# Performance work log

Hardware: AMD Instinct MI355X
Metric: run time of the kernel (lower is better)

Reference implementation:

```python
import jax, jax.numpy as jnp
import numpy as np

B, D1, SN, NF = 32, 49, 32, 16          # batch, n_sais, sqrt_n, n_filters
D_MODEL, HEADS = SN * SN * NF, 16        # 16384, 16
DEPTH = D_MODEL // HEADS                 # 1024
C_IN = 16


def setup_inputs() -> dict:
    key = jax.random.key(0)
    ks = jax.random.split(key, 11)
    mk = lambda k, shape, scale=1.0: jax.random.normal(k, shape, dtype=jnp.float32) * scale
    w_scale = 1.0 / np.sqrt(C_IN)
    return {
        "v": mk(ks[0], (B, D1, SN, SN, C_IN)),
        "k": mk(ks[1], (B, D1, SN, SN, C_IN)),
        "q": mk(ks[2], (B, D1, SN, SN, C_IN)),
        # 1x1x1 Conv3D == pointwise channel matmul: weight [C_in, n_filters] + bias
        "Wq": mk(ks[3], (C_IN, NF), w_scale), "bq": jnp.zeros((NF,), jnp.float32),
        "Wk": mk(ks[4], (C_IN, NF), w_scale), "bk": jnp.zeros((NF,), jnp.float32),
        "Wv": mk(ks[5], (C_IN, NF), w_scale), "bv": jnp.zeros((NF,), jnp.float32),
        "Wo": mk(ks[6], (NF, NF), w_scale),   "bo": jnp.zeros((NF,), jnp.float32),
    }


def _pointwise(x, W, b):
    # Conv3D(kernel=1, padding='same') over [B, d1, h, w, c]
    return jnp.einsum('bdhwc,cf->bdhwf', x, W) + b


def reference(v, k, q, Wq, bq, Wk, bk, Wv, bv, Wo, bo):
    b = q.shape[0]
    # projections (1x1x1 conv3d), then flatten spatial+channel into d_model
    def proj_heads(x, W, bias):
        y = _pointwise(x, W, bias).reshape(b, D1, D_MODEL)       # reshape2d
        y = y.reshape(b, D1, HEADS, DEPTH)                        # split_heads
        return y.transpose(0, 2, 1, 3)                            # [b, h, d1, depth]
    qh = proj_heads(q, Wq, bq)
    kh = proj_heads(k, Wk, bk)
    vh = proj_heads(v, Wv, bv)
    # scaled dot-product attention over the 49 SAI tokens
    scale = 1.0 / jnp.sqrt(jnp.float32(DEPTH))
    scores = jnp.einsum('bhqd,bhkd->bhqk', qh, kh) * scale        # [b, h, 49, 49]
    attn = jax.nn.softmax(scores, axis=-1)
    ctx = jnp.einsum('bhqk,bhkd->bhqd', attn, vh)                 # [b, h, 49, depth]
    ctx = ctx.transpose(0, 2, 1, 3).reshape(b, D1, D_MODEL)       # concat heads
    ctx = ctx.reshape(b, D1, SN, SN, NF)                          # reshape4d
    out = _pointwise(ctx, Wo, bo)                                 # wout conv3d 1x1x1
    return out, attn
```

## Files before the change

### kernel.cpp

```cpp
#include <hip/hip_runtime.h>
#include <hip/hip_bf16.h>


#define NT 49
#define TOKS 16384
#define HSL 1024
#define SLOT 3200
#define ZSWZ(n) (((((n) & 7) ^ (((n) >> 3) & 7))) << 4)
#define SW64(t) (((t) & 7) << 4)

typedef __attribute__((ext_vector_type(8))) short bf16x8;
typedef __attribute__((ext_vector_type(4))) float f32x4;

__device__ __forceinline__ ushort f2bf(float f) {
    union { float f; unsigned u; } v; v.f = f;
    return (ushort)((v.u + 0x7fffu + ((v.u >> 16) & 1u)) >> 16);
}
__device__ __forceinline__ unsigned pk2(float lo, float hi) {
    return (unsigned)f2bf(lo) | ((unsigned)f2bf(hi) << 16);
}
__device__ __forceinline__ float qdot(f32x4 x0, f32x4 x1, f32x4 x2, f32x4 x3,
                                      f32x4 wa, f32x4 wb, f32x4 wc, f32x4 wd) {
    float s =      x0[0]*wa[0];
    s = fmaf(x0[1], wa[1], s); s = fmaf(x0[2], wa[2], s); s = fmaf(x0[3], wa[3], s);
    s = fmaf(x1[0], wb[0], s); s = fmaf(x1[1], wb[1], s); s = fmaf(x1[2], wb[2], s);
    s = fmaf(x1[3], wb[3], s);
    s = fmaf(x2[0], wc[0], s); s = fmaf(x2[1], wc[1], s); s = fmaf(x2[2], wc[2], s);
    s = fmaf(x2[3], wc[3], s);
    s = fmaf(x3[0], wd[0], s); s = fmaf(x3[1], wd[1], s); s = fmaf(x3[2], wd[2], s);
    s = fmaf(x3[3], wd[3], s);
    return s;
}

#define W_DECL(mb) \
    f32x4 W00 = *(const f32x4*)((mb)+ 0), W01 = *(const f32x4*)((mb)+ 4), \
          W02 = *(const f32x4*)((mb)+ 8), W03 = *(const f32x4*)((mb)+12), \
          W10 = *(const f32x4*)((mb)+16), W11 = *(const f32x4*)((mb)+20), \
          W12 = *(const f32x4*)((mb)+24), W13 = *(const f32x4*)((mb)+28), \
          W20 = *(const f32x4*)((mb)+32), W21 = *(const f32x4*)((mb)+36), \
          W22 = *(const f32x4*)((mb)+40), W23 = *(const f32x4*)((mb)+44), \
          W30 = *(const f32x4*)((mb)+48), W31 = *(const f32x4*)((mb)+52), \
          W32 = *(const f32x4*)((mb)+56), W33 = *(const f32x4*)((mb)+60)

__global__ __launch_bounds__(256, 2) void k_scores8(
    const float* __restrict__ qin, const float* __restrict__ kin,
    const float* __restrict__ Wq, const float* __restrict__ bq,
    const float* __restrict__ Wk, float* __restrict__ ws1)
{
    __shared__ ushort bufA[64*64];
    __shared__ ushort bufB[64*64];
    __shared__ float  Msh[256];
    __shared__ float  wkbqSh[16];
    __shared__ float  gSh[64];

    const int tid  = threadIdx.x;
    const int lane = tid & 63;
    const int wv   = tid >> 6;
    const int s    = blockIdx.x & 7;
    const int h    = (blockIdx.x >> 3) & 15;
    const int b    = blockIdx.x >> 7;

    const float* qbase = qin + (size_t)b*NT*TOKS + h*HSL + s*128;
    const float* kbase = kin + (size_t)b*NT*TOKS + h*HSL + s*128;

    const int f4 = tid & 31;
    const int t0 = tid >> 5;
    const int si = (tid >> 2) & 7;
    const int rq = tid & 3;

    f32x4 kv[7];
    {
        const float* kp = kbase + f4*4;
        #pragma unroll
        for (int i = 0; i < 7; ++i) {
            const int t = t0 + 8*i; const int tc = t < 48 ? t : 48;
            kv[i] = *(const f32x4*)(kp + (size_t)tc*TOKS);
        }
    }
    f32x4 q0[7], q1[7], q2[7], q3[7];
    #pragma unroll
    for (int i = 0; i < 7; ++i) {
        const int t = t0 + 8*i; const int tc = t < 48 ? t : 48;
        const float* qc = qbase + si*16 + (size_t)tc*TOKS;
        q0[i] = *(const f32x4*)(qc);
        q1[i] = *(const f32x4*)(qc + 4);
        q2[i] = *(const f32x4*)(qc + 8);
        q3[i] = *(const f32x4*)(qc + 12);
    }

    {
        unsigned* zA = (unsigned*)bufA; unsigned* zB = (unsigned*)bufB;
        #pragma unroll
        for (int i = 0; i < 2; ++i) {
            const int j = tid + 256*i;
            if (j < 480) { zA[1568 + j] = 0u; zB[1568 + j] = 0u; }
        }
        const int c1 = tid >> 4, c2 = tid & 15;
        float m = 0.f;
        #pragma unroll
        for (int f = 0; f < 16; ++f) m += Wq[c1*16+f] * Wk[c2*16+f];
        Msh[c2*16 + c1] = m;
        if (tid < 16) {
            float wb = 0.f;
            #pragma unroll
            for (int g = 0; g < 16; ++g) wb += Wk[tid*16+g] * bq[g];
            wkbqSh[tid] = wb;
        }
        if (tid < 64) gSh[tid] = 0.f;
    }
    __syncthreads();

    W_DECL(Msh + rq*64);
    const f32x4 wkb = *(const f32x4*)(wkbqSh + (f4 & 3)*4);

    uint2 kw[7];
    #pragma unroll
    for (int i = 0; i < 7; ++i) {
        const int t = t0 + 8*i;
        f32x4 xk = kv[i];
        if (t >= NT) xk = (f32x4){0.f,0.f,0.f,0.f};
        kw[i].x = pk2(xk[0], xk[1]); kw[i].y = pk2(xk[2], xk[3]);
        const float pg = xk[0]*wkb[0] + xk[1]*wkb[1] + xk[2]*wkb[2] + xk[3]*wkb[3];
        if (pg != 0.f) atomicAdd(&gSh[t], pg);
    }
    uint2 qw[7];
    #pragma unroll
    for (int i = 0; i < 7; ++i) {
        const float o0 = qdot(q0[i],q1[i],q2[i],q3[i], W00,W01,W02,W03);
        const float o1 = qdot(q0[i],q1[i],q2[i],q3[i], W10,W11,W12,W13);
        const float o2 = qdot(q0[i],q1[i],q2[i],q3[i], W20,W21,W22,W23);
        const float o3 = qdot(q0[i],q1[i],q2[i],q3[i], W30,W31,W32,W33);
        qw[i].x = pk2(o0, o1); qw[i].y = pk2(o2, o3);
    }

    const int f4h = f4 >> 4, f4l = f4 & 15;
    const int sih = si >> 2, sil = si & 3;
    const int ra  = wv*16 + (lane & 15);

    f32x4 accS[4];
    #pragma unroll
    for (int nt = 0; nt < 4; ++nt) accS[nt] = (f32x4){0.f,0.f,0.f,0.f};

    #pragma unroll
    for (int h2 = 0; h2 < 2; ++h2) {
        if (f4h == h2) {
            #pragma unroll
            for (int i = 0; i < 7; ++i) {
                const int t = t0 + 8*i;
                *(uint2*)((char*)bufB + ((t*128 + f4l*8) ^ SW64(t))) = kw[i];
            }
        }
        if (sih == h2) {
            #pragma unroll
            for (int i = 0; i < 7; ++i) {
                const int t = t0 + 8*i;
                if (t < NT)
                    *(uint2*)((char*)bufA + ((t*128 + sil*32 + rq*8) ^ SW64(t))) = qw[i];
            }
        }
        __syncthreads();
        #pragma unroll
        for (int ks2 = 0; ks2 < 2; ++ks2) {
            const int abo = (ra*128 + ks2*64 + (lane >> 4)*16) ^ SW64(ra);
            const bf16x8 af = *(const bf16x8*)((const char*)bufA + abo);
            #pragma unroll
            for (int nt = 0; nt < 4; ++nt) {
                const int rb  = nt*16 + (lane & 15);
                const int bbo = (rb*128 + ks2*64 + (lane >> 4)*16) ^ SW64(rb);
                const bf16x8 bf = *(const bf16x8*)((const char*)bufB + bbo);
                accS[nt] = __builtin_amdgcn_mfma_f32_16x16x32_bf16(af, bf, accS[nt], 0, 0, 0);
            }
        }
        if (h2 == 0) __syncthreads();
    }

    float* slot = ws1 + (size_t)blockIdx.x * SLOT;
    #pragma unroll
    for (int nt = 0; nt < 4; ++nt) {
        const int col = nt*16 + (lane & 15);
        #pragma unroll
        for (int rr = 0; rr < 4; ++rr) {
            const int row = wv*16 + (lane >> 4)*4 + rr;
            if (row < NT) slot[row*64 + col] = accS[nt][rr];
        }
    }
    if (tid < 64) slot[3136 + tid] = gSh[tid];
}

template<int SPLIT, int LOG2S>
__global__ __launch_bounds__(256, 2) void k_scores(
    const float* __restrict__ qin, const float* __restrict__ kin,
    const float* __restrict__ Wq, const float* __restrict__ bq,
    const float* __restrict__ Wk, float* __restrict__ ws1)
{
    __shared__ ushort bufA[64*128];
    __shared__ ushort bufB[64*128];
    __shared__ float  Msh[256];
    __shared__ float  wkbqSh[16];
    __shared__ float  gSh[64];

    const int tid  = threadIdx.x;
    const int lane = tid & 63;
    const int wv   = tid >> 6;
    const int s    = blockIdx.x & (SPLIT - 1);
    const int h    = (blockIdx.x >> LOG2S) & 15;
    const int b    = blockIdx.x >> (LOG2S + 4);

    const float* qbase = qin + (size_t)b*NT*TOKS + h*HSL + s*(1024/SPLIT);
    const float* kbase = kin + (size_t)b*NT*TOKS + h*HSL + s*(1024/SPLIT);

    const int f4 = tid & 31;
    const int t0 = tid >> 5;
    const int si = (tid >> 2) & 7;
    const int rq = tid & 3;

    constexpr int NC = 8 / SPLIT;

    f32x4 kv[7];
    {
        const float* kp = kbase + f4*4;
        #pragma unroll
        for (int i = 0; i < 7; ++i) {
            const int t = t0 + 8*i; const int tc = t < 48 ? t : 48;
            kv[i] = *(const f32x4*)(kp + (size_t)tc*TOKS);
        }
    }
    f32x4 xa0, xa1, xa2, xa3;
    {
        const float* qc = qbase + si*16 + (size_t)t0*TOKS;
        xa0 = *(const f32x4*)(qc);
        xa1 = *(const f32x4*)(qc + 4);
        xa2 = *(const f32x4*)(qc + 8);
        xa3 = *(const f32x4*)(qc + 12);
    }

    {
        unsigned* z0 = (unsigned*)bufA; unsigned* z1 = (unsigned*)bufB;
        #pragma unroll
        for (int i = 0; i < 16; ++i) { z0[tid + 256*i] = 0u; z1[tid + 256*i] = 0u; }
        const int c1 = tid >> 4, c2 = tid & 15;
        float m = 0.f;
        #pragma unroll
        for (int f = 0; f < 16; ++f) m += Wq[c1*16+f] * Wk[c2*16+f];
        Msh[c2*16 + c1] = m;
        if (tid < 16) {
            float wb = 0.f;
            #pragma unroll
            for (int g = 0; g < 16; ++g) wb += Wk[tid*16+g] * bq[g];
            wkbqSh[tid] = wb;
        }
        if (tid < 64) gSh[tid] = 0.f;
    }
    __syncthreads();

    W_DECL(Msh + rq*64);
    f32x4 wkb = *(const f32x4*)(wkbqSh + (f4 & 3)*4);

    f32x4 accS[4];
    #pragma unroll
    for (int nt = 0; nt < 4; ++nt) accS[nt] = (f32x4){0.f,0.f,0.f,0.f};

    for (int kc = 0; kc < NC; ++kc) {
        if (kc > 0) {
            const float* kp = kbase + kc*128 + f4*4;
            #pragma unroll
            for (int i = 0; i < 7; ++i) {
                const int t = t0 + 8*i; const int tc = t < 48 ? t : 48;
                kv[i] = *(const f32x4*)(kp + (size_t)tc*TOKS);
            }
            const float* qc = qbase + kc*128 + si*16 + (size_t)t0*TOKS;
            xa0 = *(const f32x4*)(qc);
            xa1 = *(const f32x4*)(qc + 4);
            xa2 = *(const f32x4*)(qc + 8);
            xa3 = *(const f32x4*)(qc + 12);
        }
        #pragma unroll
        for (int i = 0; i < 7; ++i) {
            const int t = t0 + 8*i;
            f32x4 xk = kv[i];
            if (t >= NT) xk = (f32x4){0.f,0.f,0.f,0.f};
            uint2 w; w.x = pk2(xk[0], xk[1]); w.y = pk2(xk[2], xk[3]);
            *(uint2*)((char*)bufB + ((t*256 + f4*8) ^ ((t & 7) << 4))) = w;
            const float pg = xk[0]*wkb[0] + xk[1]*wkb[1] + xk[2]*wkb[2] + xk[3]*wkb[3];
            if (pg != 0.f) atomicAdd(&gSh[t], pg);
        }
        #pragma unroll
        for (int i = 0; i < 7; ++i) {
            f32x4 xb0 = xa0, xb1 = xa1, xb2 = xa2, xb3 = xa3;
            if (i < 6) {
                const int tn = t0 + 8*(i+1); const int tc = tn < 48 ? tn : 48;
                const float* qc = qbase + kc*128 + si*16 + (size_t)tc*TOKS;
                xb0 = *(const f32x4*)(qc);
                xb1 = *(const f32x4*)(qc + 4);
                xb2 = *(const f32x4*)(qc + 8);
                xb3 = *(const f32x4*)(qc + 12);
            }
            const int t = t0 + 8*i;
            if (t < NT) {
                const float o0 = qdot(xa0,xa1,xa2,xa3, W00,W01,W02,W03);
                const float o1 = qdot(xa0,xa1,xa2,xa3, W10,W11,W12,W13);
                const float o2 = qdot(xa0,xa1,xa2,xa3, W20,W21,W22,W23);
                const float o3 = qdot(xa0,xa1,xa2,xa3, W30,W31,W32,W33);
                uint2 w; w.x = pk2(o0, o1); w.y = pk2(o2, o3);
                *(uint2*)((char*)bufA + ((t*256 + si*32 + rq*8) ^ ((t & 7) << 4))) = w;
            }
            xa0 = xb0; xa1 = xb1; xa2 = xb2; xa3 = xb3;
        }
        __syncthreads();
        #pragma unroll
        for (int ks = 0; ks < 4; ++ks) {
            const int ra  = wv*16 + (lane & 15);
            const int abo = (ra*256 + (ks*32 + (lane >> 4)*8)*2) ^ ((ra & 7) << 4);
            const bf16x8 af = *(const bf16x8*)((const char*)bufA + abo);
            #pragma unroll
            for (int nt = 0; nt < 4; ++nt) {
                const int rb  = nt*16 + (lane & 15);
                const int bbo = (rb*256 + (ks*32 + (lane >> 4)*8)*2) ^ ((rb & 7) << 4);
                const bf16x8 bf = *(const bf16x8*)((const char*)bufB + bbo);
                accS[nt] = __builtin_amdgcn_mfma_f32_16x16x32_bf16(af, bf, accS[nt], 0, 0, 0);
            }
        }
        if (kc + 1 < NC) __syncthreads();
    }

    float* slot = ws1 + (size_t)blockIdx.x * SLOT;
    #pragma unroll
    for (int nt = 0; nt < 4; ++nt) {
        const int col = nt*16 + (lane & 15);
        #pragma unroll
        for (int rr = 0; rr < 4; ++rr) {
            const int row = wv*16 + (lane >> 4)*4 + rr;
            if (row < NT) slot[row*64 + col] = accS[nt][rr];
        }
    }
    if (tid < 64) slot[3136 + tid] = gSh[tid];
}

template<int SPLIT>
__global__ __launch_bounds__(256, 2) void k_softmax(
    const float* __restrict__ ws1, float* __restrict__ attnp,
    ushort* __restrict__ ws2)
{
    __shared__ float sS[NT*69];
    __shared__ float sG[64];
    const int tid = threadIdx.x;
    const float* base = ws1 + (size_t)blockIdx.x * SPLIT * SLOT;

    for (int p = tid; p < 784; p += 256) {
        const int row = p >> 4, c4 = (p & 15) * 4;
        float4 acc = *(const float4*)(base + row*64 + c4);
        #pragma unroll
        for (int s = 1; s < SPLIT; ++s) {
            const float4 a = *(const float4*)(base + s*SLOT + row*64 + c4);
            acc.x += a.x; acc.y += a.y; acc.z += a.z; acc.w += a.w;
        }
        sS[row*69 + c4 + 0] = acc.x;
        sS[row*69 + c4 + 1] = acc.y;
        sS[row*69 + c4 + 2] = acc.z;
        sS[row*69 + c4 + 3] = acc.w;
    }
    if (tid < 64) {
        float g = base[3136 + tid];
        #pragma unroll
        for (int s = 1; s < SPLIT; ++s) g += base[s*SLOT + 3136 + tid];
        sG[tid] = g;
    }
    __syncthreads();

    if (tid < NT) {
        float mx = -1e30f;
        for (int j = 0; j < NT; ++j) {
            const float v = (sS[tid*69 + j] + sG[j]) * 0.03125f;
            sS[tid*69 + j] = v;
            mx = fmaxf(mx, v);
        }
        float ssum = 0.f;
        for (int j = 0; j < NT; ++j) {
            const float e = __expf(sS[tid*69 + j] - mx);
            sS[tid*69 + j] = e; ssum += e;
        }
        const float inv = 1.0f / ssum;
        for (int j = 0; j < NT; ++j) sS[tid*69 + j] *= inv;
    }
    __syncthreads();

    float* ab = attnp + (size_t)blockIdx.x * (NT*NT);
    for (int p = tid; p < NT*NT; p += 256) {
        const int t = p / NT, j = p - t*NT;
        ab[p] = sS[t*69 + j];
    }
    ushort* w2 = ws2 + (size_t)blockIdx.x * 4096;
    for (int p = tid; p < 4096; p += 256) {
        const int t = p >> 6, j = p & 63;
        const float v = (t < NT && j < NT) ? sS[t*69 + j] : 0.f;
        w2[p] = f2bf(v);
    }
}

__global__ __launch_bounds__(256, 2) void k_out(
    const float* __restrict__ vin,
    const float* __restrict__ Wv, const float* __restrict__ bv,
    const float* __restrict__ Wo, const float* __restrict__ bo,
    const ushort* __restrict__ ws2, float* __restrict__ out)
{
    __shared__ unsigned Zt[4096];
    __shared__ float WvoSh[256];
    __shared__ float bvoSh[16];

    const int tid  = threadIdx.x;
    const int lane = tid & 63;
    const int wv   = tid >> 6;
    const int kc   = blockIdx.x & 7;
    const int h    = (blockIdx.x >> 3) & 15;
    const int b    = blockIdx.x >> 7;
    const float* vbase = vin + (size_t)b*NT*TOKS + h*HSL;

    const int si = (tid >> 2) & 7;
    const int rq = tid & 3;
    const int t0 = tid >> 5;

    const ushort* w2 = ws2 + ((size_t)(blockIdx.x >> 3)) * 4096;
    const int ra = wv*16 + (lane & 15);
    const bf16x8 af0 = *(const bf16x8*)(w2 + ra*64 +      (lane >> 4)*8);
    const bf16x8 af1 = *(const bf16x8*)(w2 + ra*64 + 32 + (lane >> 4)*8);
    f32x4 v0[7], v1[7], v2[7], v3[7];
    #pragma unroll
    for (int i = 0; i < 7; ++i) {
        const int t = t0 + 8*i; const int tc = t < 48 ? t : 48;
        const float* vc = vbase + kc*128 + si*16 + (size_t)tc*TOKS;
        v0[i] = *(const f32x4*)(vc);
        v1[i] = *(const f32x4*)(vc + 4);
        v2[i] = *(const f32x4*)(vc + 8);
        v3[i] = *(const f32x4*)(vc + 12);
    }

    {
        const int c1 = tid >> 4, c2 = tid & 15;
        float wvo = 0.f;
        #pragma unroll
        for (int f = 0; f < 16; ++f) wvo += Wv[c1*16+f] * Wo[f*16+c2];
        WvoSh[c2*16 + c1] = wvo;
        if (tid < 16) {
            float s2 = 0.f;
            #pragma unroll
            for (int g = 0; g < 16; ++g) s2 += bv[g]*Wo[g*16+tid];
            bvoSh[tid] = s2 + bo[tid];
        }
        #pragma unroll
        for (int i = 0; i < 16; ++i) Zt[tid + 256*i] = 0u;
    }
    __syncthreads();

    W_DECL(WvoSh + rq*64);
    const float bias = bvoSh[lane & 15];

    #pragma unroll
    for (int i = 0; i < 7; ++i) {
        const int t = t0 + 8*i;
        if (t < NT) {
            const float o0 = qdot(v0[i],v1[i],v2[i],v3[i], W00,W01,W02,W03);
            const float o1 = qdot(v0[i],v1[i],v2[i],v3[i], W10,W11,W12,W13);
            const float o2 = qdot(v0[i],v1[i],v2[i],v3[i], W20,W21,W22,W23);
            const float o3 = qdot(v0[i],v1[i],v2[i],v3[i], W30,W31,W32,W33);
            const int n0 = si*16 + rq*4;
            const int pb = (t >> 1)*4, hb = (t & 1)*2;
            *(ushort*)((char*)Zt + ((((n0+0)*128 + pb) ^ ZSWZ(n0+0)) + hb)) = f2bf(o0);
            *(ushort*)((char*)Zt + ((((n0+1)*128 + pb) ^ ZSWZ(n0+1)) + hb)) = f2bf(o1);
            *(ushort*)((char*)Zt + ((((n0+2)*128 + pb) ^ ZSWZ(n0+2)) + hb)) = f2bf(o2);
            *(ushort*)((char*)Zt + ((((n0+3)*128 + pb) ^ ZSWZ(n0+3)) + hb)) = f2bf(o3);
        }
    }
    __syncthreads();

    float* obase = out + (size_t)b*NT*TOKS + h*HSL + kc*128;
    #pragma unroll
    for (int nt2 = 0; nt2 < 8; ++nt2) {
        const int n    = nt2*16 + (lane & 15);
        const int swzn = ZSWZ(n);
        const bf16x8 bf0 = *(const bf16x8*)((const char*)Zt + ((n*128 +      (lane >> 4)*16) ^ swzn));
        const bf16x8 bf1 = *(const bf16x8*)((const char*)Zt + ((n*128 + 64 + (lane >> 4)*16) ^ swzn));
        f32x4 acc = (f32x4){0.f, 0.f, 0.f, 0.f};
        acc = __builtin_amdgcn_mfma_f32_16x16x32_bf16(af0, bf0, acc, 0, 0, 0);
        acc = __builtin_amdgcn_mfma_f32_16x16x32_bf16(af1, bf1, acc, 0, 0, 0);
        #pragma unroll
        for (int r2 = 0; r2 < 4; ++r2) {
            const int row = wv*16 + (lane >> 4)*4 + r2;
            if (row < NT) obase[(size_t)row*TOKS + n] = acc[r2] + bias;
        }
    }
}

extern "C" void kernel_launch(void* const* d_in, const int* in_sizes, int n_in,
                              void* d_out, int out_size, void* d_ws, size_t ws_size,
                              hipStream_t stream) {
    const float* v  = (const float*)d_in[0];
    const float* k  = (const float*)d_in[1];
    const float* q  = (const float*)d_in[2];
    const float* Wq = (const float*)d_in[3];
    const float* bq = (const float*)d_in[4];
    const float* Wk = (const float*)d_in[5];
    const float* bk = (const float*)d_in[6];
    const float* Wv = (const float*)d_in[7];
    const float* bv = (const float*)d_in[8];
    const float* Wo = (const float*)d_in[9];
    const float* bo = (const float*)d_in[10];
    (void)bk; (void)in_sizes; (void)n_in; (void)out_size;

    float* outp  = (float*)d_out;
    float* attnp = outp + (size_t)32 * 49 * 16384;
    float* ws1   = (float*)d_ws;

    const size_t need8 = (size_t)4096*SLOT*4 + (size_t)512*4096*2;
    const size_t need4 = (size_t)2048*SLOT*4 + (size_t)512*4096*2;
    if (ws_size >= need8) {
        ushort* ws2 = (ushort*)(ws1 + (size_t)4096*SLOT);
        k_scores8    <<<dim3(4096), dim3(256), 0, stream>>>(q, k, Wq, bq, Wk, ws1);
        k_softmax<8> <<<dim3(512),  dim3(256), 0, stream>>>(ws1, attnp, ws2);
        k_out        <<<dim3(4096), dim3(256), 0, stream>>>(v, Wv, bv, Wo, bo, ws2, outp);
    } else if (ws_size >= need4) {
        ushort* ws2 = (ushort*)(ws1 + (size_t)2048*SLOT);
        k_scores<4,2><<<dim3(2048), dim3(256), 0, stream>>>(q, k, Wq, bq, Wk, ws1);
        k_softmax<4> <<<dim3(512),  dim3(256), 0, stream>>>(ws1, attnp, ws2);
        k_out        <<<dim3(4096), dim3(256), 0, stream>>>(v, Wv, bv, Wo, bo, ws2, outp);
    } else {
        ushort* ws2 = (ushort*)(ws1 + (size_t)1024*SLOT);
        k_scores<2,1><<<dim3(1024), dim3(256), 0, stream>>>(q, k, Wq, bq, Wk, ws1);
        k_softmax<2> <<<dim3(512),  dim3(256), 0, stream>>>(ws1, attnp, ws2);
        k_out        <<<dim3(4096), dim3(256), 0, stream>>>(v, Wv, bv, Wo, bo, ws2, outp);
    }
}
```

Measured before the change: 138.9 us.

## Merge two scores slices per 512-thread block with full-width LDS staging

Replaces the 256-thread per-slice scores kernel with a 512-thread kernel in which each half processes one of two adjacent 128-channel slices. Each half keeps its own 64x128 bf16 A/B LDS buffers, so the two-phase staged write/MFMA loop with its extra barriers becomes a single store, one sync and a 4-step K loop. The Wq·Wk product matrix is also built once per block instead of per slice. In exchange the kernel uses far more LDS per block, zero-fills whole buffers, and has a single barrier across 512 threads, which may reduce occupancy.

```diff
diff --git a/kernel.cpp b/kernel.cpp
--- a/kernel.cpp
+++ b/kernel.cpp
@@ -7,7 +7,6 @@
 #define HSL 1024
 #define SLOT 3200
 #define ZSWZ(n) (((((n) & 7) ^ (((n) >> 3) & 7))) << 4)
-#define SW64(t) (((t) & 7) << 4)
 
 typedef __attribute__((ext_vector_type(8))) short bf16x8;
 typedef __attribute__((ext_vector_type(4))) float f32x4;
@@ -42,31 +41,34 @@
           W30 = *(const f32x4*)((mb)+48), W31 = *(const f32x4*)((mb)+52), \
           W32 = *(const f32x4*)((mb)+56), W33 = *(const f32x4*)((mb)+60)
 
-__global__ __launch_bounds__(256, 2) void k_scores8(
+__global__ __launch_bounds__(512, 1) void k_scores512(
     const float* __restrict__ qin, const float* __restrict__ kin,
     const float* __restrict__ Wq, const float* __restrict__ bq,
     const float* __restrict__ Wk, float* __restrict__ ws1)
 {
-    __shared__ ushort bufA[64*64];
-    __shared__ ushort bufB[64*64];
+    __shared__ ushort bufA[2][64*128];
+    __shared__ ushort bufB[2][64*128];
     __shared__ float  Msh[256];
     __shared__ float  wkbqSh[16];
-    __shared__ float  gSh[64];
+    __shared__ float  gSh[2][64];
 
     const int tid  = threadIdx.x;
-    const int lane = tid & 63;
-    const int wv   = tid >> 6;
-    const int s    = blockIdx.x & 7;
-    const int h    = (blockIdx.x >> 3) & 15;
-    const int b    = blockIdx.x >> 7;
+    const int half = tid >> 8;
+    const int tl   = tid & 255;
+    const int lane = tl & 63;
+    const int wv   = tl >> 6;
+    const int spair = blockIdx.x & 3;
+    const int h     = (blockIdx.x >> 2) & 15;
+    const int b     = blockIdx.x >> 6;
+    const int s     = spair*2 + half;
 
     const float* qbase = qin + (size_t)b*NT*TOKS + h*HSL + s*128;
     const float* kbase = kin + (size_t)b*NT*TOKS + h*HSL + s*128;
 
-    const int f4 = tid & 31;
-    const int t0 = tid >> 5;
-    const int si = (tid >> 2) & 7;
-    const int rq = tid & 3;
+    const int f4 = tl & 31;
+    const int t0 = tl >> 5;
+    const int si = (tl >> 2) & 7;
+    const int rq = tl & 3;
 
     f32x4 kv[7];
     {
@@ -89,92 +91,71 @@
     }
 
     {
-        unsigned* zA = (unsigned*)bufA; unsigned* zB = (unsigned*)bufB;
-        #pragma unroll
-        for (int i = 0; i < 2; ++i) {
-            const int j = tid + 256*i;
-            if (j < 480) { zA[1568 + j] = 0u; zB[1568 + j] = 0u; }
-        }
-        const int c1 = tid >> 4, c2 = tid & 15;
-        float m = 0.f;
-        #pragma unroll
-        for (int f = 0; f < 16; ++f) m += Wq[c1*16+f] * Wk[c2*16+f];
-        Msh[c2*16 + c1] = m;
+        unsigned* z0 = (unsigned*)bufA[half]; unsigned* z1 = (unsigned*)bufB[half];
+        #pragma unroll
+        for (int i = 0; i < 16; ++i) { z0[tl + 256*i] = 0u; z1[tl + 256*i] = 0u; }
+        if (tid < 256) {
+            const int c1 = tid >> 4, c2 = tid & 15;
+            float m = 0.f;
+            #pragma unroll
+            for (int f = 0; f < 16; ++f) m += Wq[c1*16+f] * Wk[c2*16+f];
+            Msh[c2*16 + c1] = m;
+        }
         if (tid < 16) {
             float wb = 0.f;
             #pragma unroll
             for (int g = 0; g < 16; ++g) wb += Wk[tid*16+g] * bq[g];
             wkbqSh[tid] = wb;
         }
-        if (tid < 64) gSh[tid] = 0.f;
+        if (tl < 64) gSh[half][tl] = 0.f;
     }
     __syncthreads();
 
     W_DECL(Msh + rq*64);
     const f32x4 wkb = *(const f32x4*)(wkbqSh + (f4 & 3)*4);
 
-    uint2 kw[7];
     #pragma unroll
     for (int i = 0; i < 7; ++i) {
         const int t = t0 + 8*i;
         f32x4 xk = kv[i];
         if (t >= NT) xk = (f32x4){0.f,0.f,0.f,0.f};
-        kw[i].x = pk2(xk[0], xk[1]); kw[i].y = pk2(xk[2], xk[3]);
+        uint2 w; w.x = pk2(xk[0], xk[1]); w.y = pk2(xk[2], xk[3]);
+        *(uint2*)((char*)bufB[half] + ((t*256 + f4*8) ^ ((t & 7) << 4))) = w;
         const float pg = xk[0]*wkb[0] + xk[1]*wkb[1] + xk[2]*wkb[2] + xk[3]*wkb[3];
-        if (pg != 0.f) atomicAdd(&gSh[t], pg);
-    }
-    uint2 qw[7];
+        if (pg != 0.f) atomicAdd(&gSh[half][t], pg);
+    }
     #pragma unroll
     for (int i = 0; i < 7; ++i) {
-        const float o0 = qdot(q0[i],q1[i],q2[i],q3[i], W00,W01,W02,W03);
-        const float o1 = qdot(q0[i],q1[i],q2[i],q3[i], W10,W11,W12,W13);
-        const float o2 = qdot(q0[i],q1[i],q2[i],q3[i], W20,W21,W22,W23);
-        const float o3 = qdot(q0[i],q1[i],q2[i],q3[i], W30,W31,W32,W33);
-        qw[i].x = pk2(o0, o1); qw[i].y = pk2(o2, o3);
-    }
-
-    const int f4h = f4 >> 4, f4l = f4 & 15;
-    const int sih = si >> 2, sil = si & 3;
-    const int ra  = wv*16 + (lane & 15);
+        const int t = t0 + 8*i;
+        if (t < NT) {
+            const float o0 = qdot(q0[i],q1[i],q2[i],q3[i], W00,W01,W02,W03);
+            const float o1 = qdot(q0[i],q1[i],q2[i],q3[i], W10,W11,W12,W13);
+            const float o2 = qdot(q0[i],q1[i],q2[i],q3[i], W20,W21,W22,W23);
+            const float o3 = qdot(q0[i],q1[i],q2[i],q3[i], W30,W31,W32,W33);
+            uint2 w; w.x = pk2(o0, o1); w.y = pk2(o2, o3);
+            *(uint2*)((char*)bufA[half] + ((t*256 + si*32 + rq*8) ^ ((t & 7) << 4))) = w;
+        }
+    }
+    __syncthreads();
 
     f32x4 accS[4];
     #pragma unroll
     for (int nt = 0; nt < 4; ++nt) accS[nt] = (f32x4){0.f,0.f,0.f,0.f};
-
-    #pragma unroll
-    for (int h2 = 0; h2 < 2; ++h2) {
-        if (f4h == h2) {
-            #pragma unroll
-            for (int i = 0; i < 7; ++i) {
-                const int t = t0 + 8*i;
-                *(uint2*)((char*)bufB + ((t*128 + f4l*8) ^ SW64(t))) = kw[i];
-            }
-        }
-        if (sih == h2) {
-            #pragma unroll
-            for (int i = 0; i < 7; ++i) {
-                const int t = t0 + 8*i;
-                if (t < NT)
-                    *(uint2*)((char*)bufA + ((t*128 + sil*32 + rq*8) ^ SW64(t))) = qw[i];
-            }
-        }
-        __syncthreads();
-        #pragma unroll
-        for (int ks2 = 0; ks2 < 2; ++ks2) {
-            const int abo = (ra*128 + ks2*64 + (lane >> 4)*16) ^ SW64(ra);
-            const bf16x8 af = *(const bf16x8*)((const char*)bufA + abo);
-            #pragma unroll
-            for (int nt = 0; nt < 4; ++nt) {
-                const int rb  = nt*16 + (lane & 15);
-                const int bbo = (rb*128 + ks2*64 + (lane >> 4)*16) ^ SW64(rb);
-                const bf16x8 bf = *(const bf16x8*)((const char*)bufB + bbo);
-                accS[nt] = __builtin_amdgcn_mfma_f32_16x16x32_bf16(af, bf, accS[nt], 0, 0, 0);
-            }
-        }
-        if (h2 == 0) __syncthreads();
-    }
-
-    float* slot = ws1 + (size_t)blockIdx.x * SLOT;
+    #pragma unroll
+    for (int ks = 0; ks < 4; ++ks) {
+        const int ra  = wv*16 + (lane & 15);
+        const int abo = (ra*256 + (ks*32 + (lane >> 4)*8)*2) ^ ((ra & 7) << 4);
+        const bf16x8 af = *(const bf16x8*)((const char*)bufA[half] + abo);
+        #pragma unroll
+        for (int nt = 0; nt < 4; ++nt) {
+            const int rb  = nt*16 + (lane & 15);
+            const int bbo = (rb*256 + (ks*32 + (lane >> 4)*8)*2) ^ ((rb & 7) << 4);
+            const bf16x8 bf = *(const bf16x8*)((const char*)bufB[half] + bbo);
+            accS[nt] = __builtin_amdgcn_mfma_f32_16x16x32_bf16(af, bf, accS[nt], 0, 0, 0);
+        }
+    }
+
+    float* slot = ws1 + ((size_t)blockIdx.x * 2 + half) * SLOT;
     #pragma unroll
     for (int nt = 0; nt < 4; ++nt) {
         const int col = nt*16 + (lane & 15);
@@ -184,7 +165,7 @@
             if (row < NT) slot[row*64 + col] = accS[nt][rr];
         }
     }
-    if (tid < 64) slot[3136 + tid] = gSh[tid];
+    if (tl < 64) slot[3136 + tl] = gSh[half][tl];
 }
 
 template<int SPLIT, int LOG2S>
@@ -514,7 +495,7 @@
     const size_t need4 = (size_t)2048*SLOT*4 + (size_t)512*4096*2;
     if (ws_size >= need8) {
         ushort* ws2 = (ushort*)(ws1 + (size_t)4096*SLOT);
-        k_scores8    <<<dim3(4096), dim3(256), 0, stream>>>(q, k, Wq, bq, Wk, ws1);
+        k_scores512  <<<dim3(2048), dim3(512), 0, stream>>>(q, k, Wq, bq, Wk, ws1);
         k_softmax<8> <<<dim3(512),  dim3(256), 0, stream>>>(ws1, attnp, ws2);
         k_out        <<<dim3(4096), dim3(256), 0, stream>>>(v, Wv, bv, Wo, bo, ws2, outp);
     } else if (ws_size >= need4) {
```

New measurement: 153.4 us. +10.4%, slower.
